# Kernel tuning notes

Hardware: AMD Instinct MI355X
Metric: run time of the kernel (lower is better)

The kernel has to match this reference:

```python
import jax, jax.numpy as jnp
import numpy as np

KERNEL_SIZE = 5
SIGMA_SPACE = 1.0
SIGMA_COLOR = 0.1
PAD = KERNEL_SIZE // 2


def make_spatial_kernel(kernel_size, sigma_space):
    r = kernel_size // 2
    coords = jnp.arange(-r, r + 1, dtype=jnp.float32)
    xx, yy = jnp.meshgrid(coords, coords, indexing='ij')
    return jnp.exp(-(xx ** 2 + yy ** 2) / (2.0 * sigma_space ** 2))  # [K, K]


def setup_inputs() -> dict:
    key = jax.random.key(0)
    x = jax.random.uniform(key, (4, 3, 512, 512), dtype=jnp.float32)
    spatial_kernel = make_spatial_kernel(KERNEL_SIZE, SIGMA_SPACE)
    sigma_color = jnp.float32(SIGMA_COLOR)
    return {"x": x, "spatial_kernel": spatial_kernel, "sigma_color": sigma_color}


def reference(x, spatial_kernel, sigma_color):
    # x: [B, C, H, W]; spatial_kernel: [K, K] (fixed buffer, computed at init)
    B, C, H, W = x.shape
    K = KERNEL_SIZE
    padded = jnp.pad(x, ((0, 0), (0, 0), (PAD, PAD), (PAD, PAD)), mode='reflect')
    # Gather KxK windows as a trailing tap axis: [B, C, H, W, K*K]
    patches = jnp.stack(
        [padded[:, :, i:i + H, j:j + W] for i in range(K) for j in range(K)],
        axis=-1,
    )
    sk = spatial_kernel.reshape(-1)  # [K*K]
    color_diff = patches - x[..., None]
    color_weight = jnp.exp(-(color_diff ** 2) / (2.0 * sigma_color ** 2))
    weight = sk * color_weight  # [B, C, H, W, K*K]
    weight = weight / (jnp.sum(weight, axis=-1, keepdims=True) + 1e-8)
    return jnp.sum(weight * patches, axis=-1)  # [B, C, H, W]
```

## Files before the change

kernel.cpp:

```cpp
#include <hip/hip_runtime.h>

constexpr int H = 512, W = 512;
constexpr int K = 5, PADR = 2;

__global__ __launch_bounds__(256) void bilateral_kernel(
    const float* __restrict__ x,
    const float* __restrict__ sk,
    const float* __restrict__ sigma_color,
    float* __restrict__ out)
{
    __shared__ float s_lsk[K * K];
    __shared__ float s_c2;

    int t = threadIdx.x;
    if (t < K * K) s_lsk[t] = __builtin_amdgcn_logf(sk[t]);
    if (t == K * K) {
        float sc = sigma_color[0];
        s_c2 = -1.4426950408889634f / (2.0f * sc * sc);
    }
    __syncthreads();

    float lsk[K * K];
#pragma unroll
    for (int k = 0; k < K * K; ++k) lsk[k] = s_lsk[k];
    float c2 = s_c2;

    int gid = blockIdx.x * 256 + t;
    int p0 = gid << 2;
    int w0 = p0 & (W - 1);
    int row = p0 >> 9;
    int h = row & (H - 1);
    int plane = row >> 9;
    const float* xp = x + (size_t)plane * (H * W);

    int hoff[K];
#pragma unroll
    for (int i = 0; i < K; ++i) {
        int hv = h + i - PADR;
        hv = (hv < 0) ? -hv : hv;
        hv = (hv >= H) ? (2 * H - 2 - hv) : hv;
        hoff[i] = hv << 9;
    }
    int wl0 = w0 - 2; wl0 = (wl0 < 0) ? -wl0 : wl0;
    int wl1 = w0 - 1; wl1 = (wl1 < 0) ? -wl1 : wl1;
    int wr0 = w0 + 4; wr0 = (wr0 >= W) ? (2 * W - 2 - wr0) : wr0;
    int wr1 = w0 + 5; wr1 = (wr1 >= W) ? (2 * W - 2 - wr1) : wr1;

    float win[K][8];
#pragma unroll
    for (int i = 0; i < K; ++i) {
        const float* rp = xp + hoff[i];
        float4 m = *(const float4*)(rp + w0);
        win[i][2] = m.x; win[i][3] = m.y; win[i][4] = m.z; win[i][5] = m.w;
        win[i][0] = rp[wl0];
        win[i][1] = rp[wl1];
        win[i][6] = rp[wr0];
        win[i][7] = rp[wr1];
    }

    float res[4];
#pragma unroll
    for (int p = 0; p < 4; ++p) {
        float cx = win[2][p + 2];
        float wsum = 0.0f, acc = 0.0f;
#pragma unroll
        for (int i = 0; i < K; ++i) {
#pragma unroll
            for (int j = 0; j < K; ++j) {
                float v = win[i][p + j];
                float d = v - cx;
                float wgt = __builtin_amdgcn_exp2f(fmaf(d * c2, d, lsk[i * K + j]));
                wsum += wgt;
                acc = fmaf(wgt, v, acc);
            }
        }
        res[p] = acc * __builtin_amdgcn_rcpf(wsum + 1e-8f);
    }

    float4 o;
    o.x = res[0]; o.y = res[1]; o.z = res[2]; o.w = res[3];
    *(float4*)(out + p0) = o;
}

extern "C" void kernel_launch(void* const* d_in, const int* in_sizes, int n_in,
                              void* d_out, int out_size, void* d_ws, size_t ws_size,
                              hipStream_t stream) {
    const float* x  = (const float*)d_in[0];
    const float* sk = (const float*)d_in[1];
    const float* sc = (const float*)d_in[2];
    float* out = (float*)d_out;

    const int total = in_sizes[0];
    const int blocks = total / (256 * 4);
    bilateral_kernel<<<blocks, 256, 0, stream>>>(x, sk, sc, out);
}
```

Before: 85.30 us.

## Precompute log spatial weights in prep kernel and pack math into v2f ops

Moves the log of the spatial kernel and the color coefficient into a separate one-block prep kernel that writes to workspace, which removes the shared-memory setup and __syncthreads from the main kernel. The main kernel reads those weights as uniform loads and computes pairs of pixels with 2-wide float vectors, so the compiler can emit packed FP32 instructions (v_pk_fma/v_pk_mul) for the subtract, multiply and FMA work. The exp2 calls stay scalar. This adds a second kernel launch and a dependency on a workspace buffer.

```diff
diff --git a/kernel.cpp b/kernel.cpp
--- a/kernel.cpp
+++ b/kernel.cpp
@@ -1,30 +1,29 @@
 #include <hip/hip_runtime.h>
+
+typedef float v2f __attribute__((ext_vector_type(2)));
 
 constexpr int H = 512, W = 512;
 constexpr int K = 5, PADR = 2;
 
+__global__ void prep_kernel(const float* __restrict__ sk,
+                            const float* __restrict__ sigma_color,
+                            float* __restrict__ lw) {
+    int t = threadIdx.x;
+    if (t < K * K) lw[t] = __builtin_amdgcn_logf(sk[t]);
+    if (t == K * K) {
+        float s = sigma_color[0];
+        lw[K * K] = -1.4426950408889634f / (2.0f * s * s);
+    }
+}
+
 __global__ __launch_bounds__(256) void bilateral_kernel(
     const float* __restrict__ x,
-    const float* __restrict__ sk,
-    const float* __restrict__ sigma_color,
+    const float* __restrict__ lw,
     float* __restrict__ out)
 {
-    __shared__ float s_lsk[K * K];
-    __shared__ float s_c2;
+    float c2 = lw[K * K];
 
     int t = threadIdx.x;
-    if (t < K * K) s_lsk[t] = __builtin_amdgcn_logf(sk[t]);
-    if (t == K * K) {
-        float sc = sigma_color[0];
-        s_c2 = -1.4426950408889634f / (2.0f * sc * sc);
-    }
-    __syncthreads();
-
-    float lsk[K * K];
-#pragma unroll
-    for (int k = 0; k < K * K; ++k) lsk[k] = s_lsk[k];
-    float c2 = s_c2;
-
     int gid = blockIdx.x * 256 + t;
     int p0 = gid << 2;
     int w0 = p0 & (W - 1);
@@ -58,27 +57,42 @@
         win[i][7] = rp[wr1];
     }
 
-    float res[4];
+    v2f cA = { win[2][2], win[2][3] };
+    v2f cB = { win[2][4], win[2][5] };
+    v2f wsA = {0.f, 0.f}, wsB = {0.f, 0.f};
+    v2f accA = {0.f, 0.f}, accB = {0.f, 0.f};
+
 #pragma unroll
-    for (int p = 0; p < 4; ++p) {
-        float cx = win[2][p + 2];
-        float wsum = 0.0f, acc = 0.0f;
+    for (int i = 0; i < K; ++i) {
 #pragma unroll
-        for (int i = 0; i < K; ++i) {
-#pragma unroll
-            for (int j = 0; j < K; ++j) {
-                float v = win[i][p + j];
-                float d = v - cx;
-                float wgt = __builtin_amdgcn_exp2f(fmaf(d * c2, d, lsk[i * K + j]));
-                wsum += wgt;
-                acc = fmaf(wgt, v, acc);
-            }
+        for (int j = 0; j < K; ++j) {
+            float lwv = lw[i * K + j];
+            v2f lsp = { lwv, lwv };
+            v2f vA = { win[i][j],     win[i][j + 1] };
+            v2f vB = { win[i][j + 2], win[i][j + 3] };
+            v2f dA = vA - cA;
+            v2f dB = vB - cB;
+            v2f aA = dA * c2;
+            v2f aB = dB * c2;
+            v2f argA = __builtin_elementwise_fma(aA, dA, lsp);
+            v2f argB = __builtin_elementwise_fma(aB, dB, lsp);
+            v2f wA, wB;
+            wA[0] = __builtin_amdgcn_exp2f(argA[0]);
+            wA[1] = __builtin_amdgcn_exp2f(argA[1]);
+            wB[0] = __builtin_amdgcn_exp2f(argB[0]);
+            wB[1] = __builtin_amdgcn_exp2f(argB[1]);
+            wsA += wA;
+            wsB += wB;
+            accA = __builtin_elementwise_fma(wA, vA, accA);
+            accB = __builtin_elementwise_fma(wB, vB, accB);
         }
-        res[p] = acc * __builtin_amdgcn_rcpf(wsum + 1e-8f);
     }
 
     float4 o;
-    o.x = res[0]; o.y = res[1]; o.z = res[2]; o.w = res[3];
+    o.x = accA[0] * __builtin_amdgcn_rcpf(wsA[0] + 1e-8f);
+    o.y = accA[1] * __builtin_amdgcn_rcpf(wsA[1] + 1e-8f);
+    o.z = accB[0] * __builtin_amdgcn_rcpf(wsB[0] + 1e-8f);
+    o.w = accB[1] * __builtin_amdgcn_rcpf(wsB[1] + 1e-8f);
     *(float4*)(out + p0) = o;
 }
 
@@ -89,8 +103,11 @@
     const float* sk = (const float*)d_in[1];
     const float* sc = (const float*)d_in[2];
     float* out = (float*)d_out;
+    float* lw  = (float*)d_ws;
+
+    prep_kernel<<<1, 64, 0, stream>>>(sk, sc, lw);
 
     const int total = in_sizes[0];
     const int blocks = total / (256 * 4);
-    bilateral_kernel<<<blocks, 256, 0, stream>>>(x, sk, sc, out);
+    bilateral_kernel<<<blocks, 256, 0, stream>>>(x, lw, out);
 }
```

Measured after the change: 83.64 us. About the same (-1.9%).

## Process eight pixels per thread with packed v2f math and readlane weights

Applied to the files above, without the earlier changes.

Each thread now computes eight horizontally adjacent outputs instead of four. The arithmetic is written in two-wide float vectors so the compiler can emit packed FMA and subtract instructions. The log spatial weights are now spread across wavefront lanes with readlane instead of going through shared memory and a barrier. This relieves VALU pressure and amortizes halo loads, but raises register use and halves the number of blocks, which may lower occupancy.

```diff
diff --git a/kernel.cpp b/kernel.cpp
--- a/kernel.cpp
+++ b/kernel.cpp
@@ -1,7 +1,15 @@
 #include <hip/hip_runtime.h>
+
+typedef float v2f __attribute__((ext_vector_type(2)));
 
 constexpr int H = 512, W = 512;
 constexpr int K = 5, PADR = 2;
+
+__device__ inline float readlane_f(float v, int l) {
+    union { float f; int i; } u; u.f = v;
+    u.i = __builtin_amdgcn_readlane(u.i, l);
+    return u.f;
+}
 
 __global__ __launch_bounds__(256) void bilateral_kernel(
     const float* __restrict__ x,
@@ -9,24 +17,21 @@
     const float* __restrict__ sigma_color,
     float* __restrict__ out)
 {
-    __shared__ float s_lsk[K * K];
-    __shared__ float s_c2;
+    int t = threadIdx.x;
+    int lane = t & 63;
 
-    int t = threadIdx.x;
-    if (t < K * K) s_lsk[t] = __builtin_amdgcn_logf(sk[t]);
-    if (t == K * K) {
-        float sc = sigma_color[0];
-        s_c2 = -1.4426950408889634f / (2.0f * sc * sc);
-    }
-    __syncthreads();
-
+    float skl = sk[lane < K * K ? lane : 0];
+    float vlog = __builtin_amdgcn_logf(skl);
     float lsk[K * K];
 #pragma unroll
-    for (int k = 0; k < K * K; ++k) lsk[k] = s_lsk[k];
-    float c2 = s_c2;
+    for (int k = 0; k < K * K; ++k) lsk[k] = readlane_f(vlog, k);
+
+    float s = sigma_color[0];
+    float c2 = -1.4426950408889634f / (2.0f * s * s);
+    v2f c2v = { c2, c2 };
 
     int gid = blockIdx.x * 256 + t;
-    int p0 = gid << 2;
+    int p0 = gid << 3;
     int w0 = p0 & (W - 1);
     int row = p0 >> 9;
     int h = row & (H - 1);
@@ -43,43 +48,63 @@
     }
     int wl0 = w0 - 2; wl0 = (wl0 < 0) ? -wl0 : wl0;
     int wl1 = w0 - 1; wl1 = (wl1 < 0) ? -wl1 : wl1;
-    int wr0 = w0 + 4; wr0 = (wr0 >= W) ? (2 * W - 2 - wr0) : wr0;
-    int wr1 = w0 + 5; wr1 = (wr1 >= W) ? (2 * W - 2 - wr1) : wr1;
+    int wr0 = w0 + 8; wr0 = (wr0 >= W) ? (2 * W - 2 - wr0) : wr0;
+    int wr1 = w0 + 9; wr1 = (wr1 >= W) ? (2 * W - 2 - wr1) : wr1;
 
-    float win[K][8];
+    float win[K][12];
 #pragma unroll
     for (int i = 0; i < K; ++i) {
         const float* rp = xp + hoff[i];
-        float4 m = *(const float4*)(rp + w0);
-        win[i][2] = m.x; win[i][3] = m.y; win[i][4] = m.z; win[i][5] = m.w;
-        win[i][0] = rp[wl0];
-        win[i][1] = rp[wl1];
-        win[i][6] = rp[wr0];
-        win[i][7] = rp[wr1];
+        float4 m0 = *(const float4*)(rp + w0);
+        float4 m1 = *(const float4*)(rp + w0 + 4);
+        win[i][2] = m0.x; win[i][3] = m0.y; win[i][4] = m0.z; win[i][5] = m0.w;
+        win[i][6] = m1.x; win[i][7] = m1.y; win[i][8] = m1.z; win[i][9] = m1.w;
+        win[i][0]  = rp[wl0];
+        win[i][1]  = rp[wl1];
+        win[i][10] = rp[wr0];
+        win[i][11] = rp[wr1];
     }
 
-    float res[4];
+    v2f cc[4], ws[4], acc[4];
 #pragma unroll
-    for (int p = 0; p < 4; ++p) {
-        float cx = win[2][p + 2];
-        float wsum = 0.0f, acc = 0.0f;
+    for (int q = 0; q < 4; ++q) {
+        cc[q][0] = win[2][2 * q + 2];
+        cc[q][1] = win[2][2 * q + 3];
+        ws[q] = (v2f){0.f, 0.f};
+        acc[q] = (v2f){0.f, 0.f};
+    }
+
 #pragma unroll
-        for (int i = 0; i < K; ++i) {
+    for (int i = 0; i < K; ++i) {
 #pragma unroll
-            for (int j = 0; j < K; ++j) {
-                float v = win[i][p + j];
-                float d = v - cx;
-                float wgt = __builtin_amdgcn_exp2f(fmaf(d * c2, d, lsk[i * K + j]));
-                wsum += wgt;
-                acc = fmaf(wgt, v, acc);
+        for (int j = 0; j < K; ++j) {
+            float lwv = lsk[i * K + j];
+            v2f lsp = { lwv, lwv };
+#pragma unroll
+            for (int q = 0; q < 4; ++q) {
+                v2f v = { win[i][2 * q + j], win[i][2 * q + j + 1] };
+                v2f d = v - cc[q];
+                v2f arg = __builtin_elementwise_fma(d * c2v, d, lsp);
+                v2f wq;
+                wq[0] = __builtin_amdgcn_exp2f(arg[0]);
+                wq[1] = __builtin_amdgcn_exp2f(arg[1]);
+                ws[q] += wq;
+                acc[q] = __builtin_elementwise_fma(wq, v, acc[q]);
             }
         }
-        res[p] = acc * __builtin_amdgcn_rcpf(wsum + 1e-8f);
     }
 
-    float4 o;
-    o.x = res[0]; o.y = res[1]; o.z = res[2]; o.w = res[3];
-    *(float4*)(out + p0) = o;
+    float4 o0, o1;
+    o0.x = acc[0][0] * __builtin_amdgcn_rcpf(ws[0][0] + 1e-8f);
+    o0.y = acc[0][1] * __builtin_amdgcn_rcpf(ws[0][1] + 1e-8f);
+    o0.z = acc[1][0] * __builtin_amdgcn_rcpf(ws[1][0] + 1e-8f);
+    o0.w = acc[1][1] * __builtin_amdgcn_rcpf(ws[1][1] + 1e-8f);
+    o1.x = acc[2][0] * __builtin_amdgcn_rcpf(ws[2][0] + 1e-8f);
+    o1.y = acc[2][1] * __builtin_amdgcn_rcpf(ws[2][1] + 1e-8f);
+    o1.z = acc[3][0] * __builtin_amdgcn_rcpf(ws[3][0] + 1e-8f);
+    o1.w = acc[3][1] * __builtin_amdgcn_rcpf(ws[3][1] + 1e-8f);
+    *(float4*)(out + p0)     = o0;
+    *(float4*)(out + p0 + 4) = o1;
 }
 
 extern "C" void kernel_launch(void* const* d_in, const int* in_sizes, int n_in,
@@ -91,6 +116,6 @@
     float* out = (float*)d_out;
 
     const int total = in_sizes[0];
-    const int blocks = total / (256 * 4);
+    const int blocks = total / (256 * 8);
     bilateral_kernel<<<blocks, 256, 0, stream>>>(x, sk, sc, out);
 }
```

New measurement: 82.83 us, median of 2. 2.9% less time.
